# Performance work log

Measured on AMD Instinct MI355X. Metric: run time of the kernel, lower is better.

## Reference

```python
import jax, jax.numpy as jnp
import numpy as np

MAX_BITS = 256.0  # 2**8


def _quantize_kernel(kern):
    # ConfigurableDense.quantize(): symmetric 8-bit fake-quantization of the kernel.
    # qmin starts at 1e10, qmax at -1e10, so first call uses min/max of kernel.
    qmin = jnp.minimum(jnp.float32(1e10), jnp.min(kern))
    qmax = jnp.maximum(jnp.float32(-1e10), jnp.max(kern))
    s = 2.0 * jnp.maximum(jnp.abs(qmin), jnp.abs(qmax)) / MAX_BITS
    return jnp.round(kern / s) * s


def setup_inputs() -> dict:
    key = jax.random.key(0)
    ks = jax.random.split(key, 9)
    B, S, D_IN, D_MODEL = 4, 2048, 1024, 1024
    sc = 0.02
    return {
        "q": jax.random.normal(ks[0], (B, S, D_IN), jnp.float32),
        "k": jax.random.normal(ks[1], (B, S, D_IN), jnp.float32),
        "v": jax.random.normal(ks[2], (B, S, D_IN), jnp.float32),
        "Wq": jax.random.normal(ks[3], (D_IN, D_MODEL), jnp.float32) * sc,
        "bq": jax.random.normal(ks[4], (D_MODEL,), jnp.float32) * sc,
        "Wk": jax.random.normal(ks[5], (D_IN, D_MODEL), jnp.float32) * sc,
        "bk": jax.random.normal(ks[6], (D_MODEL,), jnp.float32) * sc,
        "Wv": jax.random.normal(ks[7], (D_IN, D_MODEL), jnp.float32) * sc,
        "bv": jax.random.normal(ks[8], (D_MODEL,), jnp.float32) * sc,
    }


def reference(q, k, v, Wq, bq, Wk, bk, Wv, bv):
    # Projections with fake-quantized kernels (ConfigurableDense, activation=None).
    qp = jnp.einsum('bsi,id->bsd', q, _quantize_kernel(Wq)) + bq
    kp = jnp.einsum('bsi,id->bsd', k, _quantize_kernel(Wk)) + bk
    vp = jnp.einsum('bsi,id->bsd', v, _quantize_kernel(Wv)) + bv
    # MovingAverageQuantizers are identity on the first call (steps=0 < warmup).
    dk = jnp.float32(kp.shape[-1])
    logits = jnp.einsum('bqd,bkd->bqk', qp, kp) / jnp.sqrt(dk)  # [B, S, S]
    attn = jax.nn.softmax(logits, axis=-1)
    return jnp.einsum('bqk,bkd->bqd', attn, vp)
```

## Files before the change

kernel.cpp:

```cpp
#include <hip/hip_runtime.h>
#include <stdint.h>


typedef unsigned short ushort_t;
typedef __attribute__((ext_vector_type(8))) short short8;
typedef __bf16 bf16x8 __attribute__((ext_vector_type(8)));
typedef __attribute__((ext_vector_type(4))) float floatx4;
typedef __attribute__((ext_vector_type(8))) int int8v;

__device__ __forceinline__ ushort_t f2bf(float x) {
  unsigned u = __float_as_uint(x);
  unsigned r = (u + 0x7fffu + ((u >> 16) & 1u)) >> 16;
  return (ushort_t)r;
}
__device__ __forceinline__ float bf2f(ushort_t u) {
  return __uint_as_float(((unsigned)u) << 16);
}
__device__ __forceinline__ unsigned char f2fp8(float x) {
  return (unsigned char)(__builtin_amdgcn_cvt_pk_fp8_f32(x, x, 0, false) & 0xff);
}

__device__ __forceinline__ void gl_lds16(const void* g, void* l) {
  __builtin_amdgcn_global_load_lds(
      (const __attribute__((address_space(1))) unsigned int*)g,
      (__attribute__((address_space(3))) unsigned int*)l, 16, 0, 0);
}

#define BM 128
#define BN 128
#define BK 64

template <int CMODE, int SWAP>
__global__ __launch_bounds__(256, 2) void gemm_bt(
    const ushort_t* __restrict__ A, const ushort_t* __restrict__ Bt,
    void* __restrict__ Cv, void* __restrict__ Cv8,
    const float* __restrict__ bias0, const float* __restrict__ bias1,
    const float* __restrict__ bias2, int K, int ldc, float alpha, long strideA,
    long strideB, long strideC) {
  __shared__ __attribute__((aligned(16))) ushort_t sA[BM * BK];
  __shared__ __attribute__((aligned(16))) ushort_t sB[BN * BK];

  const int t = threadIdx.x;
  const int lane = t & 63;
  const int wave = t >> 6;
  const int bm = SWAP ? blockIdx.x : blockIdx.y;
  const int bn = SWAP ? blockIdx.y : blockIdx.x;
  const int bz = blockIdx.z;

  const ushort_t* Ab = A + (long)bz * strideA;
  const ushort_t* Bb = Bt + (long)bz * strideB;

  const long a_row0 = (long)bm * BM;
  const long b_row0 = (long)bn * BN;

  const int crow = t >> 3;
  const int schunk = (t & 7) ^ (crow & 7);

  const ushort_t* gA = Ab + (a_row0 + crow) * (long)K + schunk * 8;
  const ushort_t* gB = Bb + (b_row0 + crow) * (long)K + schunk * 8;

  ushort_t* lA = sA + wave * 512;
  ushort_t* lB = sB + wave * 512;

  floatx4 acc[4][4];
#pragma unroll
  for (int i = 0; i < 4; ++i)
#pragma unroll
    for (int j = 0; j < 4; ++j) acc[i][j] = {0.f, 0.f, 0.f, 0.f};

  const int wm = (wave & 1) * 64;
  const int wn = (wave >> 1) * 64;
  const int fr = lane & 15;
  const int fg = lane >> 4;

  int offA[2][4], offB[2][4];
#pragma unroll
  for (int s = 0; s < 2; ++s)
#pragma unroll
    for (int i = 0; i < 4; ++i) {
      int rowA = wm + i * 16 + fr;
      int rowB = wn + i * 16 + fr;
      int cg = s * 4 + fg;
      offA[s][i] = rowA * BK + ((cg ^ (rowA & 7)) * 8);
      offB[s][i] = rowB * BK + ((cg ^ (rowB & 7)) * 8);
    }

  for (int k0 = 0; k0 < K; k0 += BK) {
#pragma unroll
    for (int i = 0; i < 4; ++i) {
      gl_lds16(gA + (long)i * 32 * K, lA + i * 2048);
      gl_lds16(gB + (long)i * 32 * K, lB + i * 2048);
    }
    gA += BK;
    gB += BK;
    __syncthreads();

#pragma unroll
    for (int s = 0; s < 2; ++s) {
      bf16x8 af[4], bfr[4];
#pragma unroll
      for (int i = 0; i < 4; ++i) {
        af[i] = *(const bf16x8*)&sA[offA[s][i]];
        bfr[i] = *(const bf16x8*)&sB[offB[s][i]];
      }
#pragma unroll
      for (int mi = 0; mi < 4; ++mi)
#pragma unroll
        for (int ni = 0; ni < 4; ++ni)
          acc[mi][ni] = __builtin_amdgcn_mfma_f32_16x16x32_bf16(
              af[mi], bfr[ni], acc[mi][ni], 0, 0, 0);
    }
    __syncthreads();
  }

  const int r0 = fg * 4;
  const int cc = fr;
  const float* bias =
      (CMODE == 3) ? (bz == 0 ? bias0 : (bz == 1 ? bias1 : bias2)) : bias0;
  float* Cz32 = (float*)Cv + (long)bz * strideC;
  unsigned char* C8 = (unsigned char*)Cv8 + (long)bz * 8388608L;
  ushort_t* CvpT = (ushort_t*)Cv;

#pragma unroll
  for (int mi = 0; mi < 4; ++mi) {
#pragma unroll
    for (int ni = 0; ni < 4; ++ni) {
      long gm0 = a_row0 + wm + mi * 16 + r0;
      long gn = b_row0 + wn + ni * 16 + cc;
      float vv[4];
#pragma unroll
      for (int r = 0; r < 4; ++r) {
        vv[r] = acc[mi][ni][r] * alpha;
        if (bias) vv[r] += bias[gn];
      }
      if (CMODE == 2) {
#pragma unroll
        for (int r = 0; r < 4; ++r) Cz32[(gm0 + r) * ldc + gn] = vv[r];
      } else if (CMODE == 3 && bz == 2) {
        long b = gm0 >> 11, s = gm0 & 2047;
        ushort4 u4;
        u4.x = f2bf(vv[0]); u4.y = f2bf(vv[1]);
        u4.z = f2bf(vv[2]); u4.w = f2bf(vv[3]);
        *(ushort4*)&CvpT[b * (2048L * 1024L) + gn * 2048L + s] = u4;
      } else {
#pragma unroll
        for (int r = 0; r < 4; ++r) C8[(gm0 + r) * 1024 + gn] = f2fp8(vv[r]);
      }
    }
  }
}

__global__ __launch_bounds__(256, 2) void qk_fp8(
    const unsigned char* __restrict__ Q8, const unsigned char* __restrict__ K8,
    ushort_t* __restrict__ P) {
  __shared__ __attribute__((aligned(16))) unsigned char sA[128 * 128];
  __shared__ __attribute__((aligned(16))) unsigned char sB[128 * 128];
  const int t = threadIdx.x;
  const int lane = t & 63, wave = t >> 6;
  const int bm = blockIdx.x, bn = blockIdx.y, bz = blockIdx.z;

  const unsigned char* Ab = Q8 + (long)bz * 2097152L + (long)bm * 128 * 1024;
  const unsigned char* Bb = K8 + (long)bz * 2097152L + (long)bn * 128 * 1024;

  const int crow = t >> 3;
  const int schunk = (t & 7) ^ (crow & 7);
  const unsigned char* gA = Ab + crow * 1024 + schunk * 16;
  const unsigned char* gB = Bb + crow * 1024 + schunk * 16;
  unsigned char* lA = sA + wave * 1024;
  unsigned char* lB = sB + wave * 1024;

  floatx4 acc[4][4];
#pragma unroll
  for (int i = 0; i < 4; ++i)
#pragma unroll
    for (int j = 0; j < 4; ++j) acc[i][j] = {0.f, 0.f, 0.f, 0.f};

  const int wm = (wave & 1) * 64;
  const int wn = (wave >> 1) * 64;
  const int fr = lane & 15;
  const int fg = lane >> 4;

  int offA[4][2], offB[4][2];
#pragma unroll
  for (int i = 0; i < 4; ++i) {
    int rA = wm + i * 16 + fr;
    int rB = wn + i * 16 + fr;
    offA[i][0] = rA * 128 + (((2 * fg) ^ (rA & 7)) * 16);
    offA[i][1] = rA * 128 + (((2 * fg + 1) ^ (rA & 7)) * 16);
    offB[i][0] = rB * 128 + (((2 * fg) ^ (rB & 7)) * 16);
    offB[i][1] = rB * 128 + (((2 * fg + 1) ^ (rB & 7)) * 16);
  }

  for (int k0 = 0; k0 < 1024; k0 += 128) {
#pragma unroll
    for (int i = 0; i < 4; ++i) {
      gl_lds16(gA + (long)i * 32 * 1024, lA + i * 4096);
      gl_lds16(gB + (long)i * 32 * 1024, lB + i * 4096);
    }
    gA += 128;
    gB += 128;
    __syncthreads();

    int8v af[4], bfr[4];
#pragma unroll
    for (int i = 0; i < 4; ++i) {
      int4 lo = *(const int4*)&sA[offA[i][0]];
      int4 hi = *(const int4*)&sA[offA[i][1]];
      af[i][0] = lo.x; af[i][1] = lo.y; af[i][2] = lo.z; af[i][3] = lo.w;
      af[i][4] = hi.x; af[i][5] = hi.y; af[i][6] = hi.z; af[i][7] = hi.w;
      int4 lo2 = *(const int4*)&sB[offB[i][0]];
      int4 hi2 = *(const int4*)&sB[offB[i][1]];
      bfr[i][0] = lo2.x; bfr[i][1] = lo2.y; bfr[i][2] = lo2.z; bfr[i][3] = lo2.w;
      bfr[i][4] = hi2.x; bfr[i][5] = hi2.y; bfr[i][6] = hi2.z; bfr[i][7] = hi2.w;
    }
#pragma unroll
    for (int mi = 0; mi < 4; ++mi)
#pragma unroll
      for (int ni = 0; ni < 4; ++ni)
        acc[mi][ni] = __builtin_amdgcn_mfma_scale_f32_16x16x128_f8f6f4(
            af[mi], bfr[ni], acc[mi][ni], 0, 0, 0, 127, 0, 127);
    __syncthreads();
  }

  const int r0 = fg * 4;
  const int cc = fr;
#pragma unroll
  for (int mi = 0; mi < 4; ++mi)
#pragma unroll
    for (int ni = 0; ni < 4; ++ni)
#pragma unroll
      for (int r = 0; r < 4; ++r) {
        long gm = (long)bm * 128 + wm + mi * 16 + r0 + r;
        long gn = (long)bn * 128 + wn + ni * 16 + cc;
        P[(long)bz * 4194304L + gm * 2048 + gn] =
            f2bf(acc[mi][ni][r] * 0.03125f);
      }
}

__global__ __launch_bounds__(256) void absmax_k(
    const float* __restrict__ W0, const float* __restrict__ W1,
    const float* __restrict__ W2, unsigned* __restrict__ outv) {
  const float* W = blockIdx.z == 0 ? W0 : (blockIdx.z == 1 ? W1 : W2);
  float m = 0.f;
  const long n = 1024L * 1024L;
  for (long i = (long)blockIdx.x * blockDim.x + threadIdx.x; i < n;
       i += (long)gridDim.x * blockDim.x)
    m = fmaxf(m, fabsf(W[i]));
  for (int off = 32; off; off >>= 1) m = fmaxf(m, __shfl_xor(m, off));
  __shared__ float red[4];
  int lane = threadIdx.x & 63, wave = threadIdx.x >> 6;
  if (lane == 0) red[wave] = m;
  __syncthreads();
  if (threadIdx.x == 0) {
    m = fmaxf(fmaxf(red[0], red[1]), fmaxf(red[2], red[3]));
    atomicMax(&outv[blockIdx.z], __float_as_uint(m));
  }
}

__global__ __launch_bounds__(256) void quant_w_k(
    const float* __restrict__ W0, const float* __restrict__ W1,
    const float* __restrict__ W2, const unsigned* __restrict__ scales,
    ushort_t* __restrict__ Wt) {
  const int z = blockIdx.z;
  const float* W = z == 0 ? W0 : (z == 1 ? W1 : W2);
  const float s = __uint_as_float(scales[z]) * (1.0f / 128.0f);
  __shared__ float tile[32][33];
  const int tx = threadIdx.x & 31, ty = threadIdx.x >> 5;
  const int k0 = blockIdx.y * 32, n0 = blockIdx.x * 32;
#pragma unroll
  for (int i = 0; i < 4; ++i)
    tile[ty + i * 8][tx] = W[(long)(k0 + ty + i * 8) * 1024 + n0 + tx];
  __syncthreads();
  ushort_t* wt = Wt + (long)z * 1024 * 1024;
#pragma unroll
  for (int i = 0; i < 4; ++i) {
    float w = tile[tx][ty + i * 8];
    float qv = rintf(w / s) * s;
    wt[(long)(n0 + ty + i * 8) * 1024 + k0 + tx] = f2bf(qv);
  }
}

__global__ __launch_bounds__(256) void cast3_k(
    const float* __restrict__ q, const float* __restrict__ k,
    const float* __restrict__ v, ushort_t* __restrict__ qb,
    ushort_t* __restrict__ kb, ushort_t* __restrict__ vb) {
  const int z = blockIdx.z;
  const float4* src = (const float4*)(z == 0 ? q : (z == 1 ? k : v));
  ushort_t* dst = z == 0 ? qb : (z == 1 ? kb : vb);
  const long nv = (4L * 2048 * 1024) / 4;
  for (long i = (long)blockIdx.x * blockDim.x + threadIdx.x; i < nv;
       i += (long)gridDim.x * blockDim.x) {
    float4 f = src[i];
    ushort4 u4;
    u4.x = f2bf(f.x); u4.y = f2bf(f.y); u4.z = f2bf(f.z); u4.w = f2bf(f.w);
    *(ushort4*)(dst + i * 4) = u4;
  }
}

__global__ __launch_bounds__(256) void softmax_k(ushort_t* __restrict__ P) {
  const long row = blockIdx.x;
  ushort_t* p = P + row * 2048;
  const int t = threadIdx.x;
  const int lane = t & 63, wave = t >> 6;
  short8 v8 = *(const short8*)&p[t * 8];
  float x[8];
#pragma unroll
  for (int j = 0; j < 8; ++j) x[j] = bf2f((ushort_t)v8[j]);
  float m = x[0];
#pragma unroll
  for (int j = 1; j < 8; ++j) m = fmaxf(m, x[j]);
  for (int off = 32; off; off >>= 1) m = fmaxf(m, __shfl_xor(m, off));
  __shared__ float rmax[4], rsum[4];
  if (lane == 0) rmax[wave] = m;
  __syncthreads();
  m = fmaxf(fmaxf(rmax[0], rmax[1]), fmaxf(rmax[2], rmax[3]));
  float s = 0.f;
#pragma unroll
  for (int j = 0; j < 8; ++j) {
    x[j] = __expf(x[j] - m);
    s += x[j];
  }
  for (int off = 32; off; off >>= 1) s += __shfl_xor(s, off);
  if (lane == 0) rsum[wave] = s;
  __syncthreads();
  s = rsum[0] + rsum[1] + rsum[2] + rsum[3];
  float inv = 1.0f / s;
  short8 o8;
#pragma unroll
  for (int j = 0; j < 8; ++j) o8[j] = (short)f2bf(x[j] * inv);
  *(short8*)&p[t * 8] = o8;
}

extern "C" void kernel_launch(void* const* d_in, const int* in_sizes, int n_in,
                              void* d_out, int out_size, void* d_ws,
                              size_t ws_size, hipStream_t stream) {
  const float* q = (const float*)d_in[0];
  const float* k = (const float*)d_in[1];
  const float* v = (const float*)d_in[2];
  const float* Wq = (const float*)d_in[3];
  const float* bq = (const float*)d_in[4];
  const float* Wk = (const float*)d_in[5];
  const float* bk = (const float*)d_in[6];
  const float* Wv = (const float*)d_in[7];
  const float* bv = (const float*)d_in[8];
  float* out = (float*)d_out;
  char* ws = (char*)d_ws;

  unsigned* scales = (unsigned*)ws;
  ushort_t* Wt = (ushort_t*)(ws + 256);
  ushort_t* qb = (ushort_t*)(ws + 6291712);
  ushort_t* kb = qb + 8388608;
  ushort_t* vb = kb + 8388608;
  ushort_t* P = qb;
  ushort_t* vpT = (ushort_t*)(ws + 73400576);
  unsigned char* qp8 = (unsigned char*)(ws + 90177792);
  unsigned char* kp8 = (unsigned char*)(ws + 98566400);

  hipMemsetAsync(scales, 0, 64, stream);
  absmax_k<<<dim3(64, 1, 3), 256, 0, stream>>>(Wq, Wk, Wv, scales);
  quant_w_k<<<dim3(32, 32, 3), 256, 0, stream>>>(Wq, Wk, Wv, scales, Wt);
  cast3_k<<<dim3(512, 1, 3), 256, 0, stream>>>(q, k, v, qb, kb, vb);

  gemm_bt<3, 1><<<dim3(64, 8, 3), 256, 0, stream>>>(
      qb, Wt, vpT, qp8, bq, bk, bv, 1024, 1024, 1.0f, 8388608L, 1048576L, 0L);

  qk_fp8<<<dim3(16, 16, 4), 256, 0, stream>>>(qp8, kp8, P);

  softmax_k<<<8192, 256, 0, stream>>>(P);

  gemm_bt<2, 1><<<dim3(16, 8, 4), 256, 0, stream>>>(
      P, vpT, out, nullptr, nullptr, nullptr, nullptr, 2048, 1024, 1.0f,
      4194304L, 2097152L, 2097152L);
}
```

Measured before the change: 315.2 us.

## Replace projection GEMM with 256x256-tile, 8-wave, double-buffered pipelined kernel

Adds a new projection GEMM kernel for the three QKV projections. It uses 256x256 output tiles across 512 threads with double-buffered LDS filled by direct global-to-LDS loads. It interleaves quarter-tile loads with MFMA blocks under explicit waitcnt, barriers and setprio. The aim is higher data reuse per tile and overlap of memory traffic with matrix math. In exchange it uses more LDS and registers per block and launches fewer blocks (384), which risks poorer occupancy and tail effects.

After: 320.7 us. About the same (+1.7%).

```diff
diff --git a/kernel.cpp b/kernel.cpp
--- a/kernel.cpp
+++ b/kernel.cpp
@@ -24,6 +24,261 @@
   __builtin_amdgcn_global_load_lds(
       (const __attribute__((address_space(1))) unsigned int*)g,
       (__attribute__((address_space(3))) unsigned int*)l, 16, 0, 0);
+}
+
+
+#define BARRIER()                        \
+  {                                      \
+    __builtin_amdgcn_sched_barrier(0);   \
+    __builtin_amdgcn_s_barrier();        \
+    __builtin_amdgcn_sched_barrier(0);   \
+  }
+#define WAIT_LGKM0()                                  \
+  {                                                   \
+    asm volatile("s_waitcnt lgkmcnt(0)" ::: "memory"); \
+    __builtin_amdgcn_sched_barrier(0);                \
+  }
+#define WAIT_VM(n)                                         \
+  {                                                        \
+    asm volatile("s_waitcnt vmcnt(" #n ")" ::: "memory");  \
+    __builtin_amdgcn_sched_barrier(0);                     \
+  }
+
+#define STAGE_A(kt, h, buf)                                              \
+  {                                                                      \
+    gl_lds16(gA + (long)(h)*131072 + (long)(kt)*64,                      \
+             sA + (buf)*16384 + ((h)*128 + wave * 8) * 64);              \
+    gl_lds16(gA + (long)(h)*131072 + 65536 + (long)(kt)*64,              \
+             sA + (buf)*16384 + ((h)*128 + 64 + wave * 8) * 64);         \
+  }
+#define STAGE_B(kt, h, buf)                                              \
+  {                                                                      \
+    gl_lds16(gB + (long)(h)*131072 + (long)(kt)*64,                      \
+             sB + (buf)*16384 + ((h)*128 + wave * 8) * 64);              \
+    gl_lds16(gB + (long)(h)*131072 + 65536 + (long)(kt)*64,              \
+             sB + (buf)*16384 + ((h)*128 + 64 + wave * 8) * 64);         \
+  }
+
+#define RD_A(buf, qm)                                                     \
+  {                                                                       \
+    _Pragma("unroll") for (int mi = 0; mi < 4; ++mi)                      \
+        _Pragma("unroll") for (int s = 0; s < 2; ++s) aT[mi][s] =         \
+            *(const bf16x8*)&sA[(buf)*16384 + (qm)*8192 + offA[mi][s]];   \
+  }
+#define RD_B(dst, buf, qn)                                                \
+  {                                                                       \
+    _Pragma("unroll") for (int ni = 0; ni < 2; ++ni)                      \
+        _Pragma("unroll") for (int s = 0; s < 2; ++s) dst[ni][s] =        \
+            *(const bf16x8*)&sB[(buf)*16384 + (qn)*8192 + offB[ni][s]];   \
+  }
+#define MM(qm, qn, BR)                                                       \
+  {                                                                          \
+    __builtin_amdgcn_s_setprio(1);                                           \
+    _Pragma("unroll") for (int s = 0; s < 2; ++s)                            \
+        _Pragma("unroll") for (int mi = 0; mi < 4; ++mi)                     \
+            _Pragma("unroll") for (int ni = 0; ni < 2; ++ni) acc[qm][qn][mi] \
+                [ni] = __builtin_amdgcn_mfma_f32_16x16x32_bf16(              \
+                    aT[mi][s], BR[ni][s], acc[qm][qn][mi][ni], 0, 0, 0);     \
+    __builtin_amdgcn_s_setprio(0);                                           \
+  }
+
+__global__ __launch_bounds__(512, 2) void gemm256_proj(
+    const ushort_t* __restrict__ A, const ushort_t* __restrict__ Bt,
+    void* __restrict__ Cv, void* __restrict__ Cv8,
+    const float* __restrict__ bias0, const float* __restrict__ bias1,
+    const float* __restrict__ bias2) {
+  __shared__ __attribute__((aligned(16))) ushort_t sA[2 * 256 * 64];
+  __shared__ __attribute__((aligned(16))) ushort_t sB[2 * 256 * 64];
+
+  const int t = threadIdx.x;
+  const int lane = t & 63;
+  const int wave = t >> 6;
+  const int wm = wave >> 2;
+  const int wn = wave & 3;
+  const int bm = blockIdx.x;
+  const int bn = blockIdx.y;
+  const int bz = blockIdx.z;
+
+  const ushort_t* Ab = A + (long)bz * 8388608L;
+  const ushort_t* Bb = Bt + (long)bz * 1048576L;
+
+  const long a_row0 = (long)bm * 256;
+  const long b_row0 = (long)bn * 256;
+
+  const int crow = t >> 3;
+  const int schunk = (t & 7) ^ (crow & 7);
+  const ushort_t* gA = Ab + (a_row0 + crow) * 1024 + schunk * 8;
+  const ushort_t* gB = Bb + (b_row0 + crow) * 1024 + schunk * 8;
+
+  floatx4 acc[2][2][4][2];
+#pragma unroll
+  for (int a = 0; a < 2; ++a)
+#pragma unroll
+    for (int b = 0; b < 2; ++b)
+#pragma unroll
+      for (int c = 0; c < 4; ++c)
+#pragma unroll
+        for (int d = 0; d < 2; ++d) acc[a][b][c][d] = {0.f, 0.f, 0.f, 0.f};
+
+  const int fr = lane & 15;
+  const int fg = lane >> 4;
+
+  int offA[4][2], offB[2][2];
+#pragma unroll
+  for (int mi = 0; mi < 4; ++mi) {
+    int rowA = wm * 64 + mi * 16 + fr;
+#pragma unroll
+    for (int s = 0; s < 2; ++s)
+      offA[mi][s] = rowA * 64 + (((s * 4 + fg) ^ (rowA & 7)) * 8);
+  }
+#pragma unroll
+  for (int ni = 0; ni < 2; ++ni) {
+    int rowB = wn * 32 + ni * 16 + fr;
+#pragma unroll
+    for (int s = 0; s < 2; ++s)
+      offB[ni][s] = rowB * 64 + (((s * 4 + fg) ^ (rowB & 7)) * 8);
+  }
+
+  bf16x8 aT[4][2], bT0[2][2], bT1[2][2];
+
+  STAGE_A(0, 0, 0);
+  STAGE_A(0, 1, 0);
+  STAGE_B(0, 0, 0);
+  STAGE_B(0, 1, 0);
+  STAGE_A(1, 0, 1);
+  STAGE_B(1, 0, 1);
+  STAGE_B(1, 1, 1);
+  WAIT_VM(6);
+  BARRIER();
+
+#pragma unroll 1
+  for (int i = 0; i < 7; ++i) {
+    const int t0 = 2 * i;
+    RD_A(0, 0);
+    RD_B(bT0, 0, 0);
+    STAGE_A(t0 + 1, 1, 1);
+    BARRIER();
+    WAIT_LGKM0();
+    MM(0, 0, bT0);
+    BARRIER();
+    RD_B(bT1, 0, 1);
+    STAGE_A(t0 + 2, 0, 0);
+    BARRIER();
+    WAIT_LGKM0();
+    MM(0, 1, bT1);
+    BARRIER();
+    RD_A(0, 1);
+    STAGE_B(t0 + 2, 0, 0);
+    BARRIER();
+    WAIT_LGKM0();
+    MM(1, 0, bT0);
+    BARRIER();
+    STAGE_B(t0 + 2, 1, 0);
+    BARRIER();
+    WAIT_LGKM0();
+    MM(1, 1, bT1);
+    WAIT_VM(6);
+    BARRIER();
+    RD_A(1, 0);
+    RD_B(bT0, 1, 0);
+    STAGE_A(t0 + 2, 1, 0);
+    BARRIER();
+    WAIT_LGKM0();
+    MM(0, 0, bT0);
+    BARRIER();
+    RD_B(bT1, 1, 1);
+    STAGE_A(t0 + 3, 0, 1);
+    BARRIER();
+    WAIT_LGKM0();
+    MM(0, 1, bT1);
+    BARRIER();
+    RD_A(1, 1);
+    STAGE_B(t0 + 3, 0, 1);
+    BARRIER();
+    WAIT_LGKM0();
+    MM(1, 0, bT0);
+    BARRIER();
+    STAGE_B(t0 + 3, 1, 1);
+    BARRIER();
+    WAIT_LGKM0();
+    MM(1, 1, bT1);
+    WAIT_VM(6);
+    BARRIER();
+  }
+
+  RD_A(0, 0);
+  RD_B(bT0, 0, 0);
+  STAGE_A(15, 1, 1);
+  BARRIER();
+  WAIT_LGKM0();
+  MM(0, 0, bT0);
+  BARRIER();
+  RD_B(bT1, 0, 1);
+  BARRIER();
+  WAIT_LGKM0();
+  MM(0, 1, bT1);
+  BARRIER();
+  RD_A(0, 1);
+  BARRIER();
+  WAIT_LGKM0();
+  MM(1, 0, bT0);
+  BARRIER();
+  BARRIER();
+  WAIT_LGKM0();
+  MM(1, 1, bT1);
+  WAIT_VM(0);
+  BARRIER();
+  RD_A(1, 0);
+  RD_B(bT0, 1, 0);
+  BARRIER();
+  WAIT_LGKM0();
+  MM(0, 0, bT0);
+  BARRIER();
+  RD_B(bT1, 1, 1);
+  BARRIER();
+  WAIT_LGKM0();
+  MM(0, 1, bT1);
+  BARRIER();
+  RD_A(1, 1);
+  BARRIER();
+  WAIT_LGKM0();
+  MM(1, 0, bT0);
+  BARRIER();
+  WAIT_LGKM0();
+  MM(1, 1, bT1);
+
+  const int r0v = fg * 4;
+  const float* bias = (bz == 0) ? bias0 : (bz == 1 ? bias1 : bias2);
+  unsigned char* C8 = (unsigned char*)Cv8 + (long)bz * 8388608L;
+  ushort_t* CvpT = (ushort_t*)Cv;
+
+#pragma unroll
+  for (int qm = 0; qm < 2; ++qm)
+#pragma unroll
+    for (int qn = 0; qn < 2; ++qn)
+#pragma unroll
+      for (int mi = 0; mi < 4; ++mi)
+#pragma unroll
+        for (int ni = 0; ni < 2; ++ni) {
+          long gm0 = a_row0 + qm * 128 + wm * 64 + mi * 16 + r0v;
+          long gn = b_row0 + qn * 128 + wn * 32 + ni * 16 + fr;
+          float vv[4];
+#pragma unroll
+          for (int r = 0; r < 4; ++r)
+            vv[r] = acc[qm][qn][mi][ni][r] + bias[gn];
+          if (bz == 2) {
+            long b = gm0 >> 11, s = gm0 & 2047;
+            ushort4 u4;
+            u4.x = f2bf(vv[0]);
+            u4.y = f2bf(vv[1]);
+            u4.z = f2bf(vv[2]);
+            u4.w = f2bf(vv[3]);
+            *(ushort4*)&CvpT[b * (2048L * 1024L) + gn * 2048L + s] = u4;
+          } else {
+#pragma unroll
+            for (int r = 0; r < 4; ++r) C8[(gm0 + r) * 1024 + gn] = f2fp8(vv[r]);
+          }
+        }
 }
 
 #define BM 128
@@ -115,11 +370,7 @@
 
   const int r0 = fg * 4;
   const int cc = fr;
-  const float* bias =
-      (CMODE == 3) ? (bz == 0 ? bias0 : (bz == 1 ? bias1 : bias2)) : bias0;
   float* Cz32 = (float*)Cv + (long)bz * strideC;
-  unsigned char* C8 = (unsigned char*)Cv8 + (long)bz * 8388608L;
-  ushort_t* CvpT = (ushort_t*)Cv;
 
 #pragma unroll
   for (int mi = 0; mi < 4; ++mi) {
@@ -129,22 +380,10 @@
       long gn = b_row0 + wn + ni * 16 + cc;
       float vv[4];
 #pragma unroll
-      for (int r = 0; r < 4; ++r) {
-        vv[r] = acc[mi][ni][r] * alpha;
-        if (bias) vv[r] += bias[gn];
-      }
+      for (int r = 0; r < 4; ++r) vv[r] = acc[mi][ni][r] * alpha;
       if (CMODE == 2) {
 #pragma unroll
         for (int r = 0; r < 4; ++r) Cz32[(gm0 + r) * ldc + gn] = vv[r];
-      } else if (CMODE == 3 && bz == 2) {
-        long b = gm0 >> 11, s = gm0 & 2047;
-        ushort4 u4;
-        u4.x = f2bf(vv[0]); u4.y = f2bf(vv[1]);
-        u4.z = f2bf(vv[2]); u4.w = f2bf(vv[3]);
-        *(ushort4*)&CvpT[b * (2048L * 1024L) + gn * 2048L + s] = u4;
-      } else {
-#pragma unroll
-        for (int r = 0; r < 4; ++r) C8[(gm0 + r) * 1024 + gn] = f2fp8(vv[r]);
       }
     }
   }
@@ -361,8 +600,8 @@
   quant_w_k<<<dim3(32, 32, 3), 256, 0, stream>>>(Wq, Wk, Wv, scales, Wt);
   cast3_k<<<dim3(512, 1, 3), 256, 0, stream>>>(q, k, v, qb, kb, vb);
 
-  gemm_bt<3, 1><<<dim3(64, 8, 3), 256, 0, stream>>>(
-      qb, Wt, vpT, qp8, bq, bk, bv, 1024, 1024, 1.0f, 8388608L, 1048576L, 0L);
+  gemm256_proj<<<dim3(32, 4, 3), 512, 0, stream>>>(qb, Wt, vpT, qp8, bq, bk,
+                                                   bv);
 
   qk_fp8<<<dim3(16, 16, 4), 256, 0, stream>>>(qp8, kp8, P);
 
```

## Add 256x256 double-buffered 8-wave projection GEMM with interleaved staging

Applied to the files above, without the earlier changes.

Replaces the 128x128 projection GEMM for Q/K/V with a new 256x256-tile kernel using 512 threads, double-buffered LDS, and direct global-to-LDS loads interleaved with MFMA quadrants under explicit barriers and vmcnt waits. It also raises wave priority around MFMA blocks. The intent is more data reuse per tile and better overlap of memory loads with compute in the projection stage. The larger tile yields only 384 blocks, which may leave some compute units idle, and the hand-scheduled barrier pattern is fragile.

Result: no change. 317.0 us (+0.6%).

```diff
diff --git a/kernel.cpp b/kernel.cpp
--- a/kernel.cpp
+++ b/kernel.cpp
@@ -24,6 +24,220 @@
   __builtin_amdgcn_global_load_lds(
       (const __attribute__((address_space(1))) unsigned int*)g,
       (__attribute__((address_space(3))) unsigned int*)l, 16, 0, 0);
+}
+
+
+#define BARRIER()                        \
+  {                                      \
+    __builtin_amdgcn_sched_barrier(0);   \
+    __builtin_amdgcn_s_barrier();        \
+    __builtin_amdgcn_sched_barrier(0);   \
+  }
+#define WAIT_VM(n)                                         \
+  {                                                        \
+    asm volatile("s_waitcnt vmcnt(" #n ")" ::: "memory");  \
+    __builtin_amdgcn_sched_barrier(0);                     \
+  }
+
+#define STAGE_A(c, h, buf)                                           \
+  {                                                                  \
+    gl_lds16(gA + (h)*131072 + (c)*64,                               \
+             sA + (buf)*16384 + ((h)*128 + wave * 8) * 64);          \
+    gl_lds16(gA + (h)*131072 + 65536 + (c)*64,                       \
+             sA + (buf)*16384 + ((h)*128 + 64 + wave * 8) * 64);     \
+  }
+#define STAGE_B(c, h, buf)                                           \
+  {                                                                  \
+    gl_lds16(gB + (h)*131072 + (c)*64,                               \
+             sB + (buf)*16384 + ((h)*128 + wave * 8) * 64);          \
+    gl_lds16(gB + (h)*131072 + 65536 + (c)*64,                       \
+             sB + (buf)*16384 + ((h)*128 + 64 + wave * 8) * 64);     \
+  }
+
+#define RD_A(dst, buf, qm)                                                   \
+  {                                                                          \
+    _Pragma("unroll") for (int mi = 0; mi < 4; ++mi) {                       \
+      dst[mi][0] =                                                           \
+          *(const bf16x8*)&sA[(buf)*16384 + (qm)*8192 + mi * 1024 + aB0];    \
+      dst[mi][1] =                                                           \
+          *(const bf16x8*)&sA[(buf)*16384 + (qm)*8192 + mi * 1024 + aB1];    \
+    }                                                                        \
+  }
+#define RD_B(dst, buf, qn)                                                   \
+  {                                                                          \
+    _Pragma("unroll") for (int ni = 0; ni < 2; ++ni) {                       \
+      dst[ni][0] =                                                           \
+          *(const bf16x8*)&sB[(buf)*16384 + (qn)*8192 + ni * 1024 + bB0];    \
+      dst[ni][1] =                                                           \
+          *(const bf16x8*)&sB[(buf)*16384 + (qn)*8192 + ni * 1024 + bB1];    \
+    }                                                                        \
+  }
+#define MM(qm, qn, AR, BR)                                                   \
+  {                                                                          \
+    __builtin_amdgcn_s_setprio(1);                                           \
+    _Pragma("unroll") for (int s = 0; s < 2; ++s)                            \
+        _Pragma("unroll") for (int mi = 0; mi < 4; ++mi)                     \
+            _Pragma("unroll") for (int ni = 0; ni < 2; ++ni) acc[qm][qn][mi] \
+                [ni] = __builtin_amdgcn_mfma_f32_16x16x32_bf16(              \
+                    AR[mi][s], BR[ni][s], acc[qm][qn][mi][ni], 0, 0, 0);     \
+    __builtin_amdgcn_s_setprio(0);                                           \
+  }
+
+__global__ __launch_bounds__(512, 2) void gemm256_proj(
+    const ushort_t* __restrict__ A, const ushort_t* __restrict__ Bt,
+    void* __restrict__ Cv, void* __restrict__ Cv8,
+    const float* __restrict__ bias0, const float* __restrict__ bias1,
+    const float* __restrict__ bias2) {
+  __shared__ __attribute__((aligned(16))) ushort_t sA[2 * 256 * 64];
+  __shared__ __attribute__((aligned(16))) ushort_t sB[2 * 256 * 64];
+
+  const int t = threadIdx.x;
+  const int lane = t & 63;
+  const int wave = t >> 6;
+  const int wm = wave >> 2;
+  const int wn = wave & 3;
+  const int bm = blockIdx.x;
+  const int bn = blockIdx.y;
+  const int bz = blockIdx.z;
+
+  const ushort_t* Ab = A + (long)bz * 8388608L;
+  const ushort_t* Bb = Bt + (long)bz * 1048576L;
+
+  const long a_row0 = (long)bm * 256;
+  const long b_row0 = (long)bn * 256;
+
+  const int crow = t >> 3;
+  const int schunk = (t & 7) ^ (crow & 7);
+  const ushort_t* gA = Ab + (a_row0 + crow) * 1024 + schunk * 8;
+  const ushort_t* gB = Bb + (b_row0 + crow) * 1024 + schunk * 8;
+
+  floatx4 acc[2][2][4][2];
+#pragma unroll
+  for (int a = 0; a < 2; ++a)
+#pragma unroll
+    for (int b = 0; b < 2; ++b)
+#pragma unroll
+      for (int c = 0; c < 4; ++c)
+#pragma unroll
+        for (int d = 0; d < 2; ++d) acc[a][b][c][d] = {0.f, 0.f, 0.f, 0.f};
+
+  const int fr = lane & 15;
+  const int fg = lane >> 4;
+
+  const int xs0 = (fg ^ (fr & 7)) * 8;
+  const int xs1 = ((4 + fg) ^ (fr & 7)) * 8;
+  const int aB0 = (wm * 64 + fr) * 64 + xs0;
+  const int aB1 = (wm * 64 + fr) * 64 + xs1;
+  const int bB0 = (wn * 32 + fr) * 64 + xs0;
+  const int bB1 = (wn * 32 + fr) * 64 + xs1;
+
+  bf16x8 aX[4][2], aY[4][2], b0[2][2], b1[2][2];
+
+  STAGE_A(0, 0, 0);
+  STAGE_A(0, 1, 0);
+  STAGE_B(0, 0, 0);
+  STAGE_B(0, 1, 0);
+  STAGE_A(1, 0, 1);
+  STAGE_B(1, 0, 1);
+  STAGE_B(1, 1, 1);
+  WAIT_VM(6);
+  BARRIER();
+
+#pragma unroll 1
+  for (int i = 0; i < 7; ++i) {
+    STAGE_A(1, 1, 1);
+    RD_A(aX, 0, 0);
+    RD_B(b0, 0, 0);
+    RD_B(b1, 0, 1);
+    MM(0, 0, aX, b0);
+    BARRIER();
+    STAGE_A(2, 0, 0);
+    RD_A(aY, 0, 1);
+    MM(0, 1, aX, b1);
+    BARRIER();
+    STAGE_B(2, 0, 0);
+    MM(1, 0, aY, b0);
+    BARRIER();
+    STAGE_B(2, 1, 0);
+    MM(1, 1, aY, b1);
+    WAIT_VM(6);
+    BARRIER();
+    STAGE_A(2, 1, 0);
+    RD_A(aX, 1, 0);
+    RD_B(b0, 1, 0);
+    RD_B(b1, 1, 1);
+    MM(0, 0, aX, b0);
+    BARRIER();
+    STAGE_A(3, 0, 1);
+    RD_A(aY, 1, 1);
+    MM(0, 1, aX, b1);
+    BARRIER();
+    STAGE_B(3, 0, 1);
+    MM(1, 0, aY, b0);
+    BARRIER();
+    STAGE_B(3, 1, 1);
+    MM(1, 1, aY, b1);
+    WAIT_VM(6);
+    BARRIER();
+    gA += 128;
+    gB += 128;
+  }
+
+  STAGE_A(1, 1, 1);
+  RD_A(aX, 0, 0);
+  RD_B(b0, 0, 0);
+  RD_B(b1, 0, 1);
+  MM(0, 0, aX, b0);
+  BARRIER();
+  RD_A(aY, 0, 1);
+  MM(0, 1, aX, b1);
+  BARRIER();
+  MM(1, 0, aY, b0);
+  BARRIER();
+  MM(1, 1, aY, b1);
+  WAIT_VM(0);
+  BARRIER();
+  RD_A(aX, 1, 0);
+  RD_B(b0, 1, 0);
+  RD_B(b1, 1, 1);
+  MM(0, 0, aX, b0);
+  RD_A(aY, 1, 1);
+  MM(0, 1, aX, b1);
+  MM(1, 0, aY, b0);
+  MM(1, 1, aY, b1);
+
+  const int r0v = fg * 4;
+  const float* bias = (bz == 0) ? bias0 : (bz == 1 ? bias1 : bias2);
+  unsigned char* C8 = (unsigned char*)Cv8 + (long)bz * 8388608L;
+  ushort_t* CvpT = (ushort_t*)Cv;
+
+#pragma unroll
+  for (int qm = 0; qm < 2; ++qm)
+#pragma unroll
+    for (int qn = 0; qn < 2; ++qn)
+#pragma unroll
+      for (int mi = 0; mi < 4; ++mi)
+#pragma unroll
+        for (int ni = 0; ni < 2; ++ni) {
+          long gm0 = a_row0 + qm * 128 + wm * 64 + mi * 16 + r0v;
+          long gn = b_row0 + qn * 128 + wn * 32 + ni * 16 + fr;
+          float vv[4];
+#pragma unroll
+          for (int r = 0; r < 4; ++r)
+            vv[r] = acc[qm][qn][mi][ni][r] + bias[gn];
+          if (bz == 2) {
+            long b = gm0 >> 11, s = gm0 & 2047;
+            ushort4 u4;
+            u4.x = f2bf(vv[0]);
+            u4.y = f2bf(vv[1]);
+            u4.z = f2bf(vv[2]);
+            u4.w = f2bf(vv[3]);
+            *(ushort4*)&CvpT[b * (2048L * 1024L) + gn * 2048L + s] = u4;
+          } else {
+#pragma unroll
+            for (int r = 0; r < 4; ++r) C8[(gm0 + r) * 1024 + gn] = f2fp8(vv[r]);
+          }
+        }
 }
 
 #define BM 128
@@ -115,11 +329,7 @@
 
   const int r0 = fg * 4;
   const int cc = fr;
-  const float* bias =
-      (CMODE == 3) ? (bz == 0 ? bias0 : (bz == 1 ? bias1 : bias2)) : bias0;
   float* Cz32 = (float*)Cv + (long)bz * strideC;
-  unsigned char* C8 = (unsigned char*)Cv8 + (long)bz * 8388608L;
-  ushort_t* CvpT = (ushort_t*)Cv;
 
 #pragma unroll
   for (int mi = 0; mi < 4; ++mi) {
@@ -129,22 +339,10 @@
       long gn = b_row0 + wn + ni * 16 + cc;
       float vv[4];
 #pragma unroll
-      for (int r = 0; r < 4; ++r) {
-        vv[r] = acc[mi][ni][r] * alpha;
-        if (bias) vv[r] += bias[gn];
-      }
+      for (int r = 0; r < 4; ++r) vv[r] = acc[mi][ni][r] * alpha;
       if (CMODE == 2) {
 #pragma unroll
         for (int r = 0; r < 4; ++r) Cz32[(gm0 + r) * ldc + gn] = vv[r];
-      } else if (CMODE == 3 && bz == 2) {
-        long b = gm0 >> 11, s = gm0 & 2047;
-        ushort4 u4;
-        u4.x = f2bf(vv[0]); u4.y = f2bf(vv[1]);
-        u4.z = f2bf(vv[2]); u4.w = f2bf(vv[3]);
-        *(ushort4*)&CvpT[b * (2048L * 1024L) + gn * 2048L + s] = u4;
-      } else {
-#pragma unroll
-        for (int r = 0; r < 4; ++r) C8[(gm0 + r) * 1024 + gn] = f2fp8(vv[r]);
       }
     }
   }
@@ -361,8 +559,8 @@
   quant_w_k<<<dim3(32, 32, 3), 256, 0, stream>>>(Wq, Wk, Wv, scales, Wt);
   cast3_k<<<dim3(512, 1, 3), 256, 0, stream>>>(q, k, v, qb, kb, vb);
 
-  gemm_bt<3, 1><<<dim3(64, 8, 3), 256, 0, stream>>>(
-      qb, Wt, vpT, qp8, bq, bk, bv, 1024, 1024, 1.0f, 8388608L, 1048576L, 0L);
+  gemm256_proj<<<dim3(32, 4, 3), 512, 0, stream>>>(qb, Wt, vpT, qp8, bq, bk,
+                                                   bv);
 
   qk_fp8<<<dim3(16, 16, 4), 256, 0, stream>>>(qp8, kp8, P);
 
```

## Fuse fp32-to-bf16 input cast into QKV projection GEMM A-tile load

Applied to the files above, without the earlier changes.

Removes the separate cast3_k pass that converted q, k and v from fp32 to bf16 in the workspace. A new projection kernel loads fp32 A tiles straight from global memory into registers, one K-step ahead. It converts them to bf16 with v_cvt_pk_bf16_f32 and writes them swizzled into LDS, while B still streams through global_load_lds. This avoids writing and rereading 48MB of bf16 intermediates, at the cost of double the A-side global traffic inside the GEMM and register-staged loads instead of direct LDS loads.

Result: no change. 310.8 us (-1.4%).

```diff
diff --git a/kernel.cpp b/kernel.cpp
--- a/kernel.cpp
+++ b/kernel.cpp
@@ -19,11 +19,160 @@
 __device__ __forceinline__ unsigned char f2fp8(float x) {
   return (unsigned char)(__builtin_amdgcn_cvt_pk_fp8_f32(x, x, 0, false) & 0xff);
 }
+__device__ __forceinline__ int cvtpk_bf16(float a, float b) {
+  unsigned r;
+  asm("v_cvt_pk_bf16_f32 %0, %1, %2" : "=v"(r) : "v"(a), "v"(b));
+  return (int)r;
+}
 
 __device__ __forceinline__ void gl_lds16(const void* g, void* l) {
   __builtin_amdgcn_global_load_lds(
       (const __attribute__((address_space(1))) unsigned int*)g,
       (__attribute__((address_space(3))) unsigned int*)l, 16, 0, 0);
+}
+
+__global__ __launch_bounds__(256, 2) void proj_f32a(
+    const float* __restrict__ Aq, const float* __restrict__ Ak,
+    const float* __restrict__ Av, const ushort_t* __restrict__ Bt,
+    void* __restrict__ Cv, void* __restrict__ Cv8,
+    const float* __restrict__ bias0, const float* __restrict__ bias1,
+    const float* __restrict__ bias2) {
+  __shared__ __attribute__((aligned(16))) ushort_t sA[128 * 64];
+  __shared__ __attribute__((aligned(16))) ushort_t sB[128 * 64];
+
+  const int t = threadIdx.x;
+  const int lane = t & 63;
+  const int wave = t >> 6;
+  const int bm = blockIdx.x;
+  const int bn = blockIdx.y;
+  const int bz = blockIdx.z;
+
+  const float* Ab = bz == 0 ? Aq : (bz == 1 ? Ak : Av);
+  const ushort_t* Bb = Bt + (long)bz * 1048576L;
+
+  const long a_row0 = (long)bm * 128;
+  const long b_row0 = (long)bn * 128;
+
+  const int crow = t >> 3;
+  const int schunk = (t & 7) ^ (crow & 7);
+  const ushort_t* gB = Bb + (b_row0 + crow) * 1024 + schunk * 8;
+  ushort_t* lB = sB + wave * 512;
+
+  const int arow = t >> 3;
+  const int achk = t & 7;
+  const float* gA = Ab + (a_row0 + arow) * 1024 + achk * 8;
+  int awr[4];
+#pragma unroll
+  for (int k = 0; k < 4; ++k)
+    awr[k] = (k * 32 + arow) * 64 + ((achk ^ (arow & 7)) * 8);
+
+  floatx4 acc[4][4];
+#pragma unroll
+  for (int i = 0; i < 4; ++i)
+#pragma unroll
+    for (int j = 0; j < 4; ++j) acc[i][j] = {0.f, 0.f, 0.f, 0.f};
+
+  const int wm = (wave & 1) * 64;
+  const int wn = (wave >> 1) * 64;
+  const int fr = lane & 15;
+  const int fg = lane >> 4;
+
+  int offA[2][4], offB[2][4];
+#pragma unroll
+  for (int s = 0; s < 2; ++s)
+#pragma unroll
+    for (int i = 0; i < 4; ++i) {
+      int rowA = wm + i * 16 + fr;
+      int rowB = wn + i * 16 + fr;
+      int cg = s * 4 + fg;
+      offA[s][i] = rowA * 64 + ((cg ^ (rowA & 7)) * 8);
+      offB[s][i] = rowB * 64 + ((cg ^ (rowB & 7)) * 8);
+    }
+
+  float4 aL[8];
+#pragma unroll
+  for (int k = 0; k < 4; ++k) {
+    aL[2 * k] = *(const float4*)(gA + (long)k * 32 * 1024);
+    aL[2 * k + 1] = *(const float4*)(gA + (long)k * 32 * 1024 + 4);
+  }
+
+#pragma unroll 1
+  for (int k0 = 0; k0 < 1024; k0 += 64) {
+#pragma unroll
+    for (int k = 0; k < 4; ++k) {
+      int4 w;
+      w.x = cvtpk_bf16(aL[2 * k].x, aL[2 * k].y);
+      w.y = cvtpk_bf16(aL[2 * k].z, aL[2 * k].w);
+      w.z = cvtpk_bf16(aL[2 * k + 1].x, aL[2 * k + 1].y);
+      w.w = cvtpk_bf16(aL[2 * k + 1].z, aL[2 * k + 1].w);
+      *(int4*)&sA[awr[k]] = w;
+    }
+#pragma unroll
+    for (int i = 0; i < 4; ++i)
+      gl_lds16(gB + (long)i * 32 * 1024 + k0, lB + i * 2048);
+    __builtin_amdgcn_sched_barrier(0);
+    {
+      const long kn = (k0 + 64) & 1023;
+#pragma unroll
+      for (int k = 0; k < 4; ++k) {
+        aL[2 * k] = *(const float4*)(gA + (long)k * 32 * 1024 + kn);
+        aL[2 * k + 1] = *(const float4*)(gA + (long)k * 32 * 1024 + kn + 4);
+      }
+    }
+    asm volatile("s_waitcnt lgkmcnt(0) vmcnt(8)" ::: "memory");
+    __builtin_amdgcn_sched_barrier(0);
+    __builtin_amdgcn_s_barrier();
+    __builtin_amdgcn_sched_barrier(0);
+
+#pragma unroll
+    for (int s = 0; s < 2; ++s) {
+      bf16x8 af[4], bfr[4];
+#pragma unroll
+      for (int i = 0; i < 4; ++i) {
+        af[i] = *(const bf16x8*)&sA[offA[s][i]];
+        bfr[i] = *(const bf16x8*)&sB[offB[s][i]];
+      }
+#pragma unroll
+      for (int mi = 0; mi < 4; ++mi)
+#pragma unroll
+        for (int ni = 0; ni < 4; ++ni)
+          acc[mi][ni] = __builtin_amdgcn_mfma_f32_16x16x32_bf16(
+              af[mi], bfr[ni], acc[mi][ni], 0, 0, 0);
+    }
+    __builtin_amdgcn_sched_barrier(0);
+    __builtin_amdgcn_s_barrier();
+    __builtin_amdgcn_sched_barrier(0);
+  }
+
+  const int r0 = fg * 4;
+  const int cc = fr;
+  const float* bias = bz == 0 ? bias0 : (bz == 1 ? bias1 : bias2);
+  unsigned char* C8 = (unsigned char*)Cv8 + (long)bz * 8388608L;
+  ushort_t* CvpT = (ushort_t*)Cv;
+
+#pragma unroll
+  for (int mi = 0; mi < 4; ++mi) {
+#pragma unroll
+    for (int ni = 0; ni < 4; ++ni) {
+      long gm0 = a_row0 + wm + mi * 16 + r0;
+      long gn = b_row0 + wn + ni * 16 + cc;
+      float vv[4];
+#pragma unroll
+      for (int r = 0; r < 4; ++r) vv[r] = acc[mi][ni][r] + bias[gn];
+      if (bz == 2) {
+        long b = gm0 >> 11, s = gm0 & 2047;
+        ushort4 u4;
+        u4.x = f2bf(vv[0]);
+        u4.y = f2bf(vv[1]);
+        u4.z = f2bf(vv[2]);
+        u4.w = f2bf(vv[3]);
+        *(ushort4*)&CvpT[b * (2048L * 1024L) + gn * 2048L + s] = u4;
+      } else {
+#pragma unroll
+        for (int r = 0; r < 4; ++r) C8[(gm0 + r) * 1024 + gn] = f2fp8(vv[r]);
+      }
+    }
+  }
 }
 
 #define BM 128
@@ -115,11 +264,7 @@
 
   const int r0 = fg * 4;
   const int cc = fr;
-  const float* bias =
-      (CMODE == 3) ? (bz == 0 ? bias0 : (bz == 1 ? bias1 : bias2)) : bias0;
   float* Cz32 = (float*)Cv + (long)bz * strideC;
-  unsigned char* C8 = (unsigned char*)Cv8 + (long)bz * 8388608L;
-  ushort_t* CvpT = (ushort_t*)Cv;
 
 #pragma unroll
   for (int mi = 0; mi < 4; ++mi) {
@@ -129,22 +274,10 @@
       long gn = b_row0 + wn + ni * 16 + cc;
       float vv[4];
 #pragma unroll
-      for (int r = 0; r < 4; ++r) {
-        vv[r] = acc[mi][ni][r] * alpha;
-        if (bias) vv[r] += bias[gn];
-      }
+      for (int r = 0; r < 4; ++r) vv[r] = acc[mi][ni][r] * alpha;
       if (CMODE == 2) {
 #pragma unroll
         for (int r = 0; r < 4; ++r) Cz32[(gm0 + r) * ldc + gn] = vv[r];
-      } else if (CMODE == 3 && bz == 2) {
-        long b = gm0 >> 11, s = gm0 & 2047;
-        ushort4 u4;
-        u4.x = f2bf(vv[0]); u4.y = f2bf(vv[1]);
-        u4.z = f2bf(vv[2]); u4.w = f2bf(vv[3]);
-        *(ushort4*)&CvpT[b * (2048L * 1024L) + gn * 2048L + s] = u4;
-      } else {
-#pragma unroll
-        for (int r = 0; r < 4; ++r) C8[(gm0 + r) * 1024 + gn] = f2fp8(vv[r]);
       }
     }
   }
@@ -280,23 +413,6 @@
   }
 }
 
-__global__ __launch_bounds__(256) void cast3_k(
-    const float* __restrict__ q, const float* __restrict__ k,
-    const float* __restrict__ v, ushort_t* __restrict__ qb,
-    ushort_t* __restrict__ kb, ushort_t* __restrict__ vb) {
-  const int z = blockIdx.z;
-  const float4* src = (const float4*)(z == 0 ? q : (z == 1 ? k : v));
-  ushort_t* dst = z == 0 ? qb : (z == 1 ? kb : vb);
-  const long nv = (4L * 2048 * 1024) / 4;
-  for (long i = (long)blockIdx.x * blockDim.x + threadIdx.x; i < nv;
-       i += (long)gridDim.x * blockDim.x) {
-    float4 f = src[i];
-    ushort4 u4;
-    u4.x = f2bf(f.x); u4.y = f2bf(f.y); u4.z = f2bf(f.z); u4.w = f2bf(f.w);
-    *(ushort4*)(dst + i * 4) = u4;
-  }
-}
-
 __global__ __launch_bounds__(256) void softmax_k(ushort_t* __restrict__ P) {
   const long row = blockIdx.x;
   ushort_t* p = P + row * 2048;
@@ -348,10 +464,7 @@
 
   unsigned* scales = (unsigned*)ws;
   ushort_t* Wt = (ushort_t*)(ws + 256);
-  ushort_t* qb = (ushort_t*)(ws + 6291712);
-  ushort_t* kb = qb + 8388608;
-  ushort_t* vb = kb + 8388608;
-  ushort_t* P = qb;
+  ushort_t* P = (ushort_t*)(ws + 6291712);
   ushort_t* vpT = (ushort_t*)(ws + 73400576);
   unsigned char* qp8 = (unsigned char*)(ws + 90177792);
   unsigned char* kp8 = (unsigned char*)(ws + 98566400);
@@ -359,10 +472,9 @@
   hipMemsetAsync(scales, 0, 64, stream);
   absmax_k<<<dim3(64, 1, 3), 256, 0, stream>>>(Wq, Wk, Wv, scales);
   quant_w_k<<<dim3(32, 32, 3), 256, 0, stream>>>(Wq, Wk, Wv, scales, Wt);
-  cast3_k<<<dim3(512, 1, 3), 256, 0, stream>>>(q, k, v, qb, kb, vb);
-
-  gemm_bt<3, 1><<<dim3(64, 8, 3), 256, 0, stream>>>(
-      qb, Wt, vpT, qp8, bq, bk, bv, 1024, 1024, 1.0f, 8388608L, 1048576L, 0L);
+
+  proj_f32a<<<dim3(64, 8, 3), 256, 0, stream>>>(q, k, v, Wt, vpT, qp8, bq, bk,
+                                                bv);
 
   qk_fp8<<<dim3(16, 16, 4), 256, 0, stream>>>(qp8, kp8, P);
 
```
